# Performance work log

Measured on AMD Instinct MI355X. Metric: run time of the kernel, lower is better.

Reference implementation:

```python
import jax, jax.numpy as jnp
import numpy as np
import math

NUM_HEADS = 8

def setup_inputs() -> dict:
    key = jax.random.key(0)
    k1, k2, k3 = jax.random.split(key, 3)
    B, N, C = 16, 4096, 512
    x = jax.random.normal(k1, (B, N, C), dtype=jnp.float32)
    qkv_w = jax.random.normal(k2, (3 * C, C), dtype=jnp.float32) * 0.02
    proj_w = jax.random.normal(k3, (C, C), dtype=jnp.float32) * 0.02
    proj_b = jnp.zeros((C,), dtype=jnp.float32)
    return {"x": x, "qkv_w": qkv_w, "proj_w": proj_w, "proj_b": proj_b}


def reference(x, qkv_w, proj_w, proj_b):
    # Attention with is_mask=1: row-wise windowed attention.
    B, N, C = x.shape
    H = W = int(math.isqrt(N))
    nh = NUM_HEADS
    hd = C // nh
    scale = hd ** (-0.5)

    # fold rows into batch: (B*H, W, C)
    img = x.reshape(B * H, W, C)
    # qkv linear (no bias): (B*H, W, 3C) -> (3, B*H, nh, W, hd)
    qkv = jnp.einsum('bwc,dc->bwd', img, qkv_w)
    qkv = qkv.reshape(B * H, W, 3, nh, hd).transpose(2, 0, 3, 1, 4)
    q, k, v = qkv[0], qkv[1], qkv[2]

    # scaled dot-product attention within each row window
    attn = jnp.einsum('bhqd,bhkd->bhqk', q, k) * scale
    attn = jax.nn.softmax(attn, axis=-1)
    out = jnp.einsum('bhqk,bhkd->bhqd', attn, v)   # (B*H, nh, W, hd)
    out = out.transpose(0, 2, 1, 3).reshape(B, N, C)

    # output projection
    return jnp.einsum('bnc,dc->bnd', out, proj_w) + proj_b
```

## Files before the change

kernel.cpp:

```cpp
#include <hip/hip_runtime.h>
#include <cstdint>
#include <cstddef>

typedef _Float16 half8 __attribute__((ext_vector_type(8)));
typedef _Float16 half4 __attribute__((ext_vector_type(4)));
typedef float f32x4 __attribute__((ext_vector_type(4)));

#define GLDS16(g, l) __builtin_amdgcn_global_load_lds( \
    (__attribute__((address_space(1))) void*)(g), \
    (__attribute__((address_space(3))) void*)(l), 16, 0, 0)

#define LBAR() do { asm volatile("s_waitcnt lgkmcnt(0)" ::: "memory"); \
                    __builtin_amdgcn_s_barrier(); } while (0)

__global__ __launch_bounds__(256) void cvt_f32_f16(const float* __restrict__ src,
                                                   _Float16* __restrict__ dst, int n) {
  int i = (blockIdx.x * 256 + threadIdx.x) * 8;
  if (i >= n) return;
  float4 a = *(const float4*)(src + i);
  float4 b = *(const float4*)(src + i + 4);
  half8 h;
  h[0] = (_Float16)a.x; h[1] = (_Float16)a.y; h[2] = (_Float16)a.z; h[3] = (_Float16)a.w;
  h[4] = (_Float16)b.x; h[5] = (_Float16)b.y; h[6] = (_Float16)b.z; h[7] = (_Float16)b.w;
  *(half8*)(dst + i) = h;
}

template<int NOUT, int NT, bool BIAS>
__global__ __launch_bounds__(256, 2) void gemm_wide(const _Float16* __restrict__ A,
                                                    const _Float16* __restrict__ Bw,
                                                    const float* __restrict__ bias,
                                                    void* __restrict__ Cout) {
  constexpr int K = 512;
  constexpr int NIT = K / 32;
  __shared__ union {
    _Float16 S[3][12288];
    float E[2][16][132];
  } u;
  const int id  = blockIdx.x;
  const int xcd = id & 7;
  const int jj  = id >> 3;
  const int by  = (jj / NT) * 8 + xcd;
  const int bx  = jj % NT;
  const int m_base = by * 256, n_base = bx * 128;

  const int t    = threadIdx.x;
  const int lane = t & 63;
  const int wid  = t >> 6;
  const int wm   = wid >> 1;
  const int wn   = wid & 1;
  const int cl   = lane & 15, q = lane >> 4;

  f32x4 acc[8][4] = {};

  const _Float16* aP[4];
  const _Float16* bP[2];
#pragma unroll
  for (int i = 0; i < 4; ++i) {
    const int s = t + i * 256;
    const int r = ((s >> 6) << 4) | (s & 15), ch = (s >> 4) & 3;
    aP[i] = A + (size_t)(m_base + r) * K + ch * 8;
  }
#pragma unroll
  for (int i = 0; i < 2; ++i) {
    const int s = t + i * 256;
    const int r = ((s >> 6) << 4) | (s & 15), ch = (s >> 4) & 3;
    bP[i] = Bw + (size_t)(n_base + r) * K + ch * 8;
  }
  auto stage = [&](int kt) {
    const int p = kt % 3;
    const int ko = kt * 32;
    char* base = (char*)&u.S[p][0];
#pragma unroll
    for (int i = 0; i < 4; ++i)
      GLDS16(aP[i] + ko, base + (t + i * 256) * 16);
#pragma unroll
    for (int i = 0; i < 2; ++i)
      GLDS16(bP[i] + ko, base + 16384 + (t + i * 256) * 16);
  };

  stage(0);
  stage(1);

  const int lane8 = lane * 8;
#pragma unroll
  for (int k = 0; k < NIT; ++k) {
    if (k < NIT - 1) asm volatile("s_waitcnt vmcnt(6)" ::: "memory");
    else             asm volatile("s_waitcnt vmcnt(0)" ::: "memory");
    __builtin_amdgcn_s_barrier();
    asm volatile("" ::: "memory");
    if (k + 2 < NIT) stage(k + 2);

    const _Float16* As = &u.S[k % 3][0];
    const _Float16* Bs = &u.S[k % 3][8192];
    half8 af[8], bf[4];
#pragma unroll
    for (int fm = 0; fm < 8; ++fm)
      af[fm] = *(const half8*)(As + (wm * 8 + fm) * 512 + lane8);
#pragma unroll
    for (int fn = 0; fn < 4; ++fn)
      bf[fn] = *(const half8*)(Bs + (wn * 4 + fn) * 512 + lane8);
    __builtin_amdgcn_s_setprio(1);
#pragma unroll
    for (int fm = 0; fm < 8; ++fm)
#pragma unroll
      for (int fn = 0; fn < 4; ++fn)
        acc[fm][fn] = __builtin_amdgcn_mfma_f32_16x16x32_f16(af[fm], bf[fn],
                                                             acc[fm][fn], 0, 0, 0);
    __builtin_amdgcn_s_setprio(0);
    __builtin_amdgcn_s_barrier();
  }
  __syncthreads();

  const int eb = t >> 7, erow = (t >> 3) & 15, ecs = t & 7;
#pragma unroll
  for (int j = 0; j < 8; ++j) {
#pragma unroll
    for (int fn = 0; fn < 4; ++fn)
#pragma unroll
      for (int r = 0; r < 4; ++r)
        u.E[wm][q * 4 + r][wn * 64 + fn * 16 + cl] = acc[j][fn][r];
    LBAR();
    const size_t rg = (size_t)(m_base + eb * 128 + j * 16 + erow);
#pragma unroll
    for (int jo = 0; jo < 4; ++jo) {
      const int ch = ((ecs - erow) & 7) + 8 * jo;
      const int cc = ch * 4;
      float4 e = *(const float4*)&u.E[eb][erow][cc];
      if constexpr (BIAS) {
        const float4 bb = *(const float4*)(bias + n_base + cc);
        e.x += bb.x; e.y += bb.y; e.z += bb.z; e.w += bb.w;
        *(float4*)((float*)Cout + rg * NOUT + n_base + cc) = e;
      } else {
        half4 hv;
        hv[0] = (_Float16)e.x; hv[1] = (_Float16)e.y;
        hv[2] = (_Float16)e.z; hv[3] = (_Float16)e.w;
        *(half4*)((_Float16*)Cout + rg * NOUT + n_base + cc) = hv;
      }
    }
    LBAR();
  }
}

__global__ __launch_bounds__(256, 4) void attn_win(const _Float16* __restrict__ QKV,
                                                   _Float16* __restrict__ Out) {
  __shared__ _Float16 Ks[4096];
  __shared__ _Float16 Vt[64][72];
  __shared__ _Float16 Ps[64][72];
  __shared__ _Float16 Os[64][72];
  const int h = blockIdx.x, b = blockIdx.y;
  const int t = threadIdx.x;
  const int lane = t & 63, wid = t >> 6;
  const int cl = lane & 15, q = lane >> 4;
  const int m0 = wid * 16;
  const int lane8 = lane * 8;

  {
    const int s0 = t, s1 = t + 256;
    const int r0 = ((s0 >> 7) << 4) | (s0 & 15), ch0 = (s0 >> 4) & 7;
    const int r1 = ((s1 >> 7) << 4) | (s1 & 15), ch1 = (s1 >> 4) & 7;
    const _Float16* g0 = QKV + (size_t)(b * 64 + r0) * 1536 + 512 + h * 64 + ch0 * 8;
    const _Float16* g1 = QKV + (size_t)(b * 64 + r1) * 1536 + 512 + h * 64 + ch1 * 8;
    GLDS16(g0, (char*)Ks + s0 * 16);
    GLDS16(g1, (char*)Ks + s1 * 16);

    const int vj = t & 63, vp = t >> 6;
    const _Float16* vsrc = QKV + (size_t)(b * 64 + vj) * 1536 + 1024 + h * 64 + vp * 16;
    half8 v0 = *(const half8*)vsrc;
    half8 v1 = *(const half8*)(vsrc + 8);
#pragma unroll
    for (int i = 0; i < 8; i++) Vt[vp * 16 + i][vj] = v0[i];
#pragma unroll
    for (int i = 0; i < 8; i++) Vt[vp * 16 + 8 + i][vj] = v1[i];
  }

  const _Float16* qsrc = QKV + (size_t)(b * 64 + m0 + cl) * 1536 + h * 64 + q * 8;
  half8 qa0 = *(const half8*)qsrc;
  half8 qa1 = *(const half8*)(qsrc + 32);

  __syncthreads();

  f32x4 s[4] = {};
#pragma unroll
  for (int nt = 0; nt < 4; nt++) {
    half8 b0 = *(const half8*)(Ks + nt * 1024 + lane8);
    half8 b1 = *(const half8*)(Ks + nt * 1024 + 512 + lane8);
    s[nt] = __builtin_amdgcn_mfma_f32_16x16x32_f16(qa0, b0, s[nt], 0, 0, 0);
    s[nt] = __builtin_amdgcn_mfma_f32_16x16x32_f16(qa1, b1, s[nt], 0, 0, 0);
  }

  constexpr float SC = 0.125f * 1.44269504088896340736f;
#pragma unroll
  for (int r = 0; r < 4; r++) {
    float mx = fmaxf(fmaxf(s[0][r], s[1][r]), fmaxf(s[2][r], s[3][r]));
    mx = fmaxf(mx, __shfl_xor(mx, 1));
    mx = fmaxf(mx, __shfl_xor(mx, 2));
    mx = fmaxf(mx, __shfl_xor(mx, 4));
    mx = fmaxf(mx, __shfl_xor(mx, 8));
    float e[4], ssum = 0.f;
#pragma unroll
    for (int nt = 0; nt < 4; nt++) { e[nt] = exp2f((s[nt][r] - mx) * SC); ssum += e[nt]; }
    ssum += __shfl_xor(ssum, 1);
    ssum += __shfl_xor(ssum, 2);
    ssum += __shfl_xor(ssum, 4);
    ssum += __shfl_xor(ssum, 8);
    float inv = 1.f / ssum;
    const int row = m0 + q * 4 + r;
#pragma unroll
    for (int nt = 0; nt < 4; nt++) Ps[row][nt * 16 + cl] = (_Float16)(e[nt] * inv);
  }
  __syncthreads();

  f32x4 o[4] = {};
#pragma unroll
  for (int ks = 0; ks < 2; ks++) {
    half8 a = *(const half8*)&Ps[m0 + cl][ks * 32 + q * 8];
#pragma unroll
    for (int nt = 0; nt < 4; nt++) {
      half8 bb = *(const half8*)&Vt[nt * 16 + cl][ks * 32 + q * 8];
      o[nt] = __builtin_amdgcn_mfma_f32_16x16x32_f16(a, bb, o[nt], 0, 0, 0);
    }
  }
#pragma unroll
  for (int nt = 0; nt < 4; nt++)
#pragma unroll
    for (int r = 0; r < 4; r++)
      Os[m0 + q * 4 + r][nt * 16 + cl] = (_Float16)o[nt][r];
  __syncthreads();

  {
    const int row = t >> 2, cs = t & 3;
    half8 h0 = *(const half8*)&Os[row][cs * 16];
    half8 h1 = *(const half8*)&Os[row][cs * 16 + 8];
    _Float16* dst = Out + (size_t)(b * 64 + row) * 512 + h * 64 + cs * 16;
    *(half8*)dst = h0;
    *((half8*)dst + 1) = h1;
  }
}

extern "C" void kernel_launch(void* const* d_in, const int* in_sizes, int n_in,
                              void* d_out, int out_size, void* d_ws, size_t ws_size,
                              hipStream_t stream) {
  const float* x      = (const float*)d_in[0];
  const float* qkv_w  = (const float*)d_in[1];
  const float* proj_w = (const float*)d_in[2];
  const float* proj_b = (const float*)d_in[3];
  float* out = (float*)d_out;

  char* ws = (char*)d_ws;
  _Float16* QKVh = (_Float16*)ws;
  _Float16* Xh   = (_Float16*)(ws + 201326592);
  _Float16* Outh = Xh;
  _Float16* Wq   = (_Float16*)(ws + 268435456);
  _Float16* Wp   = (_Float16*)(ws + 270008320);

  cvt_f32_f16<<<16384, 256, 0, stream>>>(x, Xh, 16 * 4096 * 512);
  cvt_f32_f16<<<384, 256, 0, stream>>>(qkv_w, Wq, 1536 * 512);
  cvt_f32_f16<<<128, 256, 0, stream>>>(proj_w, Wp, 512 * 512);
  gemm_wide<1536, 12, false><<<3072, 256, 0, stream>>>(Xh, Wq, nullptr, QKVh);
  attn_win<<<dim3(8, 1024), 256, 0, stream>>>(QKVh, Outh);
  gemm_wide<512, 4, true><<<1024, 256, 0, stream>>>(Outh, Wp, proj_b, out);
}
```

Measured before the change: 493.0 us.

## Keep A row panel resident in LDS and stream weight tiles across N

Replaces the 256x128-tile GEMM with a persistent-row kernel. Each 512-thread block loads a full 128x512 A panel into LDS once, then loops over all output column tiles while double-buffering 128x32 weight slices. The previous tile's accumulators are written out a few elements per k-step, interleaved with the MFMAs of the current tile, to hide the epilogue. This removes repeated A reloads and the separate LDS epilogue, at the cost of large LDS use (one block per CU), scalar uncoalesced stores, and fewer waves per block for latency hiding.

```diff
diff --git a/kernel.cpp b/kernel.cpp
--- a/kernel.cpp
+++ b/kernel.cpp
@@ -10,8 +10,8 @@
     (__attribute__((address_space(1))) void*)(g), \
     (__attribute__((address_space(3))) void*)(l), 16, 0, 0)
 
-#define LBAR() do { asm volatile("s_waitcnt lgkmcnt(0)" ::: "memory"); \
-                    __builtin_amdgcn_s_barrier(); } while (0)
+#define FENCE() asm volatile("" ::: "memory")
+#define WAITV(n) asm volatile("s_waitcnt vmcnt(" #n ")" ::: "memory")
 
 __global__ __launch_bounds__(256) void cvt_f32_f16(const float* __restrict__ src,
                                                    _Float16* __restrict__ dst, int n) {
@@ -25,120 +25,144 @@
   *(half8*)(dst + i) = h;
 }
 
-template<int NOUT, int NT, bool BIAS>
-__global__ __launch_bounds__(256, 2) void gemm_wide(const _Float16* __restrict__ A,
-                                                    const _Float16* __restrict__ Bw,
-                                                    const float* __restrict__ bias,
-                                                    void* __restrict__ Cout) {
+template<int NOUT, int NBX, bool BIAS>
+__global__ __launch_bounds__(512, 1) void gemm_pa(const _Float16* __restrict__ A,
+                                                  const _Float16* __restrict__ Bw,
+                                                  const float* __restrict__ bias,
+                                                  void* __restrict__ Cout) {
   constexpr int K = 512;
-  constexpr int NIT = K / 32;
-  __shared__ union {
-    _Float16 S[3][12288];
-    float E[2][16][132];
-  } u;
-  const int id  = blockIdx.x;
-  const int xcd = id & 7;
-  const int jj  = id >> 3;
-  const int by  = (jj / NT) * 8 + xcd;
-  const int bx  = jj % NT;
-  const int m_base = by * 256, n_base = bx * 128;
+  __shared__ _Float16 As[65536];
+  __shared__ _Float16 Bs[2][4096];
+  __shared__ float BiasL[BIAS ? 512 : 4];
 
   const int t    = threadIdx.x;
   const int lane = t & 63;
   const int wid  = t >> 6;
-  const int wm   = wid >> 1;
-  const int wn   = wid & 1;
+  const int wm   = wid >> 2;
+  const int wn   = wid & 3;
   const int cl   = lane & 15, q = lane >> 4;
-
-  f32x4 acc[8][4] = {};
-
-  const _Float16* aP[4];
-  const _Float16* bP[2];
-#pragma unroll
-  for (int i = 0; i < 4; ++i) {
-    const int s = t + i * 256;
-    const int r = ((s >> 6) << 4) | (s & 15), ch = (s >> 4) & 3;
-    aP[i] = A + (size_t)(m_base + r) * K + ch * 8;
-  }
-#pragma unroll
-  for (int i = 0; i < 2; ++i) {
-    const int s = t + i * 256;
-    const int r = ((s >> 6) << 4) | (s & 15), ch = (s >> 4) & 3;
-    bP[i] = Bw + (size_t)(n_base + r) * K + ch * 8;
-  }
-  auto stage = [&](int kt) {
-    const int p = kt % 3;
-    const int ko = kt * 32;
-    char* base = (char*)&u.S[p][0];
-#pragma unroll
-    for (int i = 0; i < 4; ++i)
-      GLDS16(aP[i] + ko, base + (t + i * 256) * 16);
-#pragma unroll
-    for (int i = 0; i < 2; ++i)
-      GLDS16(bP[i] + ko, base + 16384 + (t + i * 256) * 16);
-  };
-
-  stage(0);
-  stage(1);
-
-  const int lane8 = lane * 8;
-#pragma unroll
-  for (int k = 0; k < NIT; ++k) {
-    if (k < NIT - 1) asm volatile("s_waitcnt vmcnt(6)" ::: "memory");
-    else             asm volatile("s_waitcnt vmcnt(0)" ::: "memory");
-    __builtin_amdgcn_s_barrier();
-    asm volatile("" ::: "memory");
-    if (k + 2 < NIT) stage(k + 2);
-
-    const _Float16* As = &u.S[k % 3][0];
-    const _Float16* Bs = &u.S[k % 3][8192];
-    half8 af[8], bf[4];
-#pragma unroll
-    for (int fm = 0; fm < 8; ++fm)
-      af[fm] = *(const half8*)(As + (wm * 8 + fm) * 512 + lane8);
-#pragma unroll
-    for (int fn = 0; fn < 4; ++fn)
-      bf[fn] = *(const half8*)(Bs + (wn * 4 + fn) * 512 + lane8);
-    __builtin_amdgcn_s_setprio(1);
-#pragma unroll
-    for (int fm = 0; fm < 8; ++fm)
-#pragma unroll
-      for (int fn = 0; fn < 4; ++fn)
-        acc[fm][fn] = __builtin_amdgcn_mfma_f32_16x16x32_f16(af[fm], bf[fn],
-                                                             acc[fm][fn], 0, 0, 0);
-    __builtin_amdgcn_s_setprio(0);
-    __builtin_amdgcn_s_barrier();
-  }
-  __syncthreads();
-
-  const int eb = t >> 7, erow = (t >> 3) & 15, ecs = t & 7;
-#pragma unroll
-  for (int j = 0; j < 8; ++j) {
-#pragma unroll
-    for (int fn = 0; fn < 4; ++fn)
-#pragma unroll
-      for (int r = 0; r < 4; ++r)
-        u.E[wm][q * 4 + r][wn * 64 + fn * 16 + cl] = acc[j][fn][r];
-    LBAR();
-    const size_t rg = (size_t)(m_base + eb * 128 + j * 16 + erow);
-#pragma unroll
-    for (int jo = 0; jo < 4; ++jo) {
-      const int ch = ((ecs - erow) & 7) + 8 * jo;
-      const int cc = ch * 4;
-      float4 e = *(const float4*)&u.E[eb][erow][cc];
+  const int m_base = blockIdx.x * 128;
+
+  const _Float16* bRow = Bw + (size_t)(((t >> 6) << 4) | (t & 15)) * K + ((t >> 4) & 3) * 8;
+
+  if constexpr (BIAS) {
+    float4 bv = *(const float4*)(bias + (t & 127) * 4);
+    if (t < 128) *(float4*)&BiasL[t * 4] = bv;
+  }
+
+#pragma unroll
+  for (int i = 0; i < 16; ++i) {
+    const int s = t + i * 512;
+    const int r = s & 15, c = (s >> 4) & 3, kt = (s >> 6) & 15, b = s >> 10;
+    GLDS16(A + (size_t)(m_base + b * 16 + r) * K + kt * 32 + c * 8, (char*)As + s * 16);
+  }
+  GLDS16(bRow, (char*)&Bs[0][0] + t * 16);
+  FENCE();
+
+  f32x4 accC[4][2] = {};
+  f32x4 accP[4][2] = {};
+  float biasP0 = 0.f, biasP1 = 0.f;
+
+  const int rowb = m_base + wm * 64 + q * 4;
+  const int colb = wn * 32 + cl;
+
+  for (int bx = 0; bx < NBX; ++bx) {
+#pragma unroll
+    for (int kt = 0; kt < 16; ++kt) {
+      if (kt < 15) {
+        GLDS16(bRow + (size_t)bx * 128 * K + (kt + 1) * 32,
+               (char*)&Bs[(kt + 1) & 1][0] + t * 16);
+      } else if (bx < NBX - 1) {
+        GLDS16(bRow + (size_t)(bx + 1) * 128 * K,
+               (char*)&Bs[0][0] + t * 16);
+      }
+      FENCE();
+      if (kt == 15) {
+        if (bx == NBX - 1) { WAITV(0); } else { WAITV(1); }
+      } else if (kt >= 1 && kt <= 11) {
+        if (bx > 0) { WAITV(4); } else { WAITV(1); }
+      } else {
+        WAITV(1);
+      }
+      __builtin_amdgcn_s_barrier();
+      FENCE();
+
+      half8 af[4], bf[2];
+#pragma unroll
+      for (int mt = 0; mt < 4; ++mt)
+        af[mt] = *(const half8*)((const char*)As + (wm * 4 + mt) * 16384 + kt * 1024 + lane * 16);
+#pragma unroll
+      for (int fn = 0; fn < 2; ++fn)
+        bf[fn] = *(const half8*)((const char*)&Bs[kt & 1][0] + (wn * 2 + fn) * 1024 + lane * 16);
+      __builtin_amdgcn_s_setprio(1);
+#pragma unroll
+      for (int mt = 0; mt < 4; ++mt)
+#pragma unroll
+        for (int fn = 0; fn < 2; ++fn)
+          accC[mt][fn] = __builtin_amdgcn_mfma_f32_16x16x32_f16(af[mt], bf[fn],
+                                                                accC[mt][fn], 0, 0, 0);
+      __builtin_amdgcn_s_setprio(0);
+      __builtin_amdgcn_s_barrier();
+      FENCE();
+
+      if (kt <= 10 && bx > 0) {
+#pragma unroll
+        for (int s2 = 0; s2 < 3; ++s2) {
+          constexpr int base_j = 0;
+          const int j = kt * 3 + s2;
+          if (j < 32) {
+            const int mt = j >> 3, fn = (j >> 2) & 1, r = j & 3;
+            const size_t row = (size_t)(rowb + mt * 16 + r);
+            const size_t col = (size_t)((bx - 1) * 128 + colb + fn * 16);
+            float v = accP[mt][fn][r];
+            if constexpr (BIAS) {
+              v += (fn ? biasP1 : biasP0);
+              ((float*)Cout)[row * NOUT + col] = v;
+            } else {
+              ((_Float16*)Cout)[row * NOUT + col] = (_Float16)v;
+            }
+          }
+          (void)base_j;
+        }
+      }
+      FENCE();
+    }
+    if (bx < NBX - 1) {
+#pragma unroll
+      for (int mt = 0; mt < 4; ++mt)
+#pragma unroll
+        for (int fn = 0; fn < 2; ++fn) {
+          accP[mt][fn] = accC[mt][fn];
+          accC[mt][fn] = f32x4{0.f, 0.f, 0.f, 0.f};
+        }
       if constexpr (BIAS) {
-        const float4 bb = *(const float4*)(bias + n_base + cc);
-        e.x += bb.x; e.y += bb.y; e.z += bb.z; e.w += bb.w;
-        *(float4*)((float*)Cout + rg * NOUT + n_base + cc) = e;
-      } else {
-        half4 hv;
-        hv[0] = (_Float16)e.x; hv[1] = (_Float16)e.y;
-        hv[2] = (_Float16)e.z; hv[3] = (_Float16)e.w;
-        *(half4*)((_Float16*)Cout + rg * NOUT + n_base + cc) = hv;
+        biasP0 = BiasL[bx * 128 + wn * 32 + cl];
+        biasP1 = BiasL[bx * 128 + wn * 32 + 16 + cl];
       }
     }
-    LBAR();
-  }
+  }
+
+  float biasC0 = 0.f, biasC1 = 0.f;
+  if constexpr (BIAS) {
+    biasC0 = BiasL[(NBX - 1) * 128 + wn * 32 + cl];
+    biasC1 = BiasL[(NBX - 1) * 128 + wn * 32 + 16 + cl];
+  }
+#pragma unroll
+  for (int mt = 0; mt < 4; ++mt)
+#pragma unroll
+    for (int fn = 0; fn < 2; ++fn)
+#pragma unroll
+      for (int r = 0; r < 4; ++r) {
+        const size_t row = (size_t)(rowb + mt * 16 + r);
+        const size_t col = (size_t)((NBX - 1) * 128 + colb + fn * 16);
+        float v = accC[mt][fn][r];
+        if constexpr (BIAS) {
+          v += (fn ? biasC1 : biasC0);
+          ((float*)Cout)[row * NOUT + col] = v;
+        } else {
+          ((_Float16*)Cout)[row * NOUT + col] = (_Float16)v;
+        }
+      }
 }
 
 __global__ __launch_bounds__(256, 4) void attn_win(const _Float16* __restrict__ QKV,
@@ -256,7 +280,7 @@
   cvt_f32_f16<<<16384, 256, 0, stream>>>(x, Xh, 16 * 4096 * 512);
   cvt_f32_f16<<<384, 256, 0, stream>>>(qkv_w, Wq, 1536 * 512);
   cvt_f32_f16<<<128, 256, 0, stream>>>(proj_w, Wp, 512 * 512);
-  gemm_wide<1536, 12, false><<<3072, 256, 0, stream>>>(Xh, Wq, nullptr, QKVh);
+  gemm_pa<1536, 12, false><<<512, 512, 0, stream>>>(Xh, Wq, nullptr, QKVh);
   attn_win<<<dim3(8, 1024), 256, 0, stream>>>(QKVh, Outh);
-  gemm_wide<512, 4, true><<<1024, 256, 0, stream>>>(Outh, Wp, proj_b, out);
-}
+  gemm_pa<512, 4, true><<<512, 512, 0, stream>>>(Outh, Wp, proj_b, out);
+}
```

Result: slower. 558.5 us (+13.3%).
